# Kernel tuning notes

Hardware: AMD Instinct MI355X
Metric: run time of the kernel (lower is better)

## Reference

```python
import jax, jax.numpy as jnp
import numpy as np

P = 4            # parallel_layers
OUT_PER = 1024   # out_features // parallel_layers
IN_F = 4096
OUT_F = 4096
EPS = 1e-6


def setup_inputs() -> dict:
    key = jax.random.key(0)
    ks = jax.random.split(key, 7)
    x = jax.random.normal(ks[0], (4, 2048, IN_F), dtype=jnp.float32)
    vq_weight = jax.random.normal(ks[1], (16384, P, 32), dtype=jnp.float32)
    w_dec = jax.random.normal(ks[2], (P, 32, 256), dtype=jnp.float32) * 0.05
    b_dec = jax.random.normal(ks[3], (P, 256), dtype=jnp.float32) * 0.01
    d_mean = jax.random.normal(ks[4], (P, 1), dtype=jnp.float32) * 0.01
    d_std = jax.random.uniform(ks[5], (P, 1), dtype=jnp.float32, minval=0.01, maxval=0.05)
    bias = jax.random.normal(ks[6], (OUT_F,), dtype=jnp.float32) * 0.02
    return {"x": x, "vq_weight": vq_weight, "w_dec": w_dec, "b_dec": b_dec,
            "d_mean": d_mean, "d_std": d_std, "bias": bias}


def reference(x, vq_weight, w_dec, b_dec, d_mean, d_std, bias):
    # Decoder (fused per-parallel-layer linear): (N,P,L) x (P,L,C) -> (N,P,C)
    stacked = jnp.einsum('npl,plc->npc', vq_weight, w_dec) + b_dec[None, :, :]
    # recover_weight: permute(1,0,2) -> (P, N, C) -> flatten -> denormalize
    w_flat = jnp.transpose(stacked, (1, 0, 2)).reshape(P, -1)
    w_flat = w_flat * (d_std + EPS) + d_mean
    # reshape to (P, out_per, in_features) -> (out_features, in_features)
    w_recon = w_flat.reshape(P, OUT_PER, IN_F).reshape(OUT_F, IN_F)
    # F.linear(x, w_recon, bias)
    out = jnp.einsum('bsi,oi->bso', x, w_recon) + bias
    return out
```

## Files before the change

kernel.cpp:

```cpp
#include <hip/hip_runtime.h>
#include <stdint.h>

#define M_DIM 8192
#define IN_F  4096
#define OUT_F 4096
#define P_LAY 4


typedef __attribute__((ext_vector_type(8))) short short8;
typedef __attribute__((ext_vector_type(4))) float f32x4;

__device__ inline unsigned short f2bf(float f) {
    unsigned int u = __builtin_bit_cast(unsigned int, f);
    u += 0x7fffu + ((u >> 16) & 1u);
    return (unsigned short)(u >> 16);
}

__global__ __launch_bounds__(256)
void prep_tables(const float* __restrict__ vq, const float* __restrict__ wdec,
                 const float* __restrict__ bdec,
                 unsigned short* __restrict__ vqh,
                 unsigned short* __restrict__ wdech) {
    const int b = blockIdx.x;
    if (b < 2048) {
        const int o4  = (b * 256 + threadIdx.x) * 4;
        const int p   = o4 >> 19;
        const int t   = (o4 >> 9) & 1023;
        const int l   = (o4 >> 4) & 31;
        const int i80 = o4 & 15;
        ushort4 pk;
        pk.x = f2bf(vq[((size_t)(t * 16 + i80 + 0) * 4 + p) * 32 + l]);
        pk.y = f2bf(vq[((size_t)(t * 16 + i80 + 1) * 4 + p) * 32 + l]);
        pk.z = f2bf(vq[((size_t)(t * 16 + i80 + 2) * 4 + p) * 32 + l]);
        pk.w = f2bf(vq[((size_t)(t * 16 + i80 + 3) * 4 + p) * 32 + l]);
        *(ushort4*)(vqh + o4) = pk;
    } else {
        const int g4 = ((b - 2048) * 256 + threadIdx.x) * 4;
        const int n  = g4 >> 8;
        const int c0 = g4 & 255;
        float v[4];
        #pragma unroll
        for (int jj = 0; jj < 4; jj++) {
            if      (n < 128)  v[jj] = wdec[g4 + jj];
            else if (n < 132)  v[jj] = bdec[(n - 128) * 256 + c0 + jj];
            else if (n == 132) v[jj] = 1.0f;
            else               v[jj] = 0.0f;
        }
        ushort4 pk;
        pk.x = f2bf(v[0]); pk.y = f2bf(v[1]); pk.z = f2bf(v[2]); pk.w = f2bf(v[3]);
        *(ushort4*)(wdech + g4) = pk;
    }
}

__global__ __launch_bounds__(256)
void gen_y(const float* __restrict__ x, const unsigned short* __restrict__ wdech,
           const float* __restrict__ dmean, const float* __restrict__ dstd,
           unsigned short* __restrict__ y,
           float* __restrict__ rowterm) {
    const int tid  = threadIdx.x;
    const int lane = tid & 63;
    const int wave = tid >> 6;
    const int s = blockIdx.x * 4 + wave;

    const float* xr = x + (size_t)s * IN_F + (lane & 15) * 256 + (lane >> 4) * 8;
    short8 a[8];
    #pragma unroll
    for (int kc = 0; kc < 8; kc++) {
        float4 u = *(const float4*)(xr + kc * 32);
        float4 v = *(const float4*)(xr + kc * 32 + 4);
        short8 t;
        t[0] = (short)f2bf(u.x); t[1] = (short)f2bf(u.y);
        t[2] = (short)f2bf(u.z); t[3] = (short)f2bf(u.w);
        t[4] = (short)f2bf(v.x); t[5] = (short)f2bf(v.y);
        t[6] = (short)f2bf(v.z); t[7] = (short)f2bf(v.w);
        a[kc] = t;
    }

    const unsigned short* wrow = wdech + (lane & 15) * 256 + (lane >> 4) * 8;
    f32x4 acc[9] = {};
    #pragma unroll
    for (int kc = 0; kc < 8; kc++) {
        #pragma unroll
        for (int nt = 0; nt < 9; nt++) {
            short8 bfr = *(const short8*)(wrow + nt * 16 * 256 + kc * 32);
            acc[nt] = __builtin_amdgcn_mfma_f32_16x16x32_bf16(a[kc], bfr, acc[nt], 0, 0, 0);
        }
    }

    #pragma unroll
    for (int nt = 0; nt < 8; nt++) {
        ushort4 pk;
        pk.x = f2bf(acc[nt][0]); pk.y = f2bf(acc[nt][1]);
        pk.z = f2bf(acc[nt][2]); pk.w = f2bf(acc[nt][3]);
        const size_t off = ((size_t)((nt >> 1) * M_DIM + s) * 512)
                         + (nt & 1) * 256 + (lane & 15) * 16 + (lane >> 4) * 4;
        *(ushort4*)(y + off) = pk;
    }
    float cs = acc[8][0] + acc[8][1] + acc[8][2] + acc[8][3];
    cs += __shfl_xor(cs, 16);
    cs += __shfl_xor(cs, 32);
    const float xsum = __shfl(cs, 4);
    if (lane < 4)
        rowterm[s * 4 + lane] = (dstd[lane] + 1e-6f) * cs + dmean[lane] * xsum;
}

__device__ inline void async16(const void* g, void* l) {
    __builtin_amdgcn_global_load_lds(
        (const __attribute__((address_space(1))) void*)g,
        (__attribute__((address_space(3))) void*)l, 16, 0, 0);
}

__global__ __launch_bounds__(256, 4)
void gemm_y(const unsigned short* __restrict__ Y,
            const unsigned short* __restrict__ V,
            const float* __restrict__ rowterm,
            const float* __restrict__ dstd,
            const float* __restrict__ bias,
            float* __restrict__ C) {
    __shared__ __attribute__((aligned(16))) unsigned short sA[2 * 128 * 32];
    __shared__ __attribute__((aligned(16))) unsigned short sB[2 * 128 * 32];

    const int tid  = threadIdx.x;
    const int lane = tid & 63;
    const int wave = tid >> 6;
    const int wm = (wave >> 1) * 64;
    const int wn = (wave & 1) * 64;

    const int m0 = blockIdx.x * 128;
    const int n0 = blockIdx.y * 128;
    const int p  = n0 >> 10;
    const int t0 = n0 & 1023;

    const char* gAb = (const char*)(Y + (size_t)p * M_DIM * 512);
    const char* gBb = (const char*)(V + (size_t)p * 1024  * 512);

    f32x4 acc[4][4] = {};
    for (int k0 = 0; k0 < 512; k0 += 64) {
        __syncthreads();
        #pragma unroll
        for (int q = 0; q < 4; q++) {
            const int u      = wave * 4 + q;
            const int kc     = u >> 3;
            const int rowblk = (u & 7) * 16;
            const int row    = rowblk + (lane >> 2);
            const int cb     = (lane & 3) * 16;
            const size_t gofs = (size_t)k0 * 2 + kc * 64 + cb;
            char* ldst = (char*)sA + kc * 8192 + rowblk * 64 + lane * 16;
            async16(gAb + (size_t)(m0 + row) * 1024 + gofs, ldst);
            ldst = (char*)sB + kc * 8192 + rowblk * 64 + lane * 16;
            async16(gBb + (size_t)(t0 + row) * 1024 + gofs, ldst);
        }
        __syncthreads();

        #pragma unroll
        for (int kc = 0; kc < 2; kc++) {
            short8 bv[4];
            #pragma unroll
            for (int ni = 0; ni < 4; ni++)
                bv[ni] = *(const short8*)((const char*)sB + kc * 8192
                        + (wn + ni * 16 + (lane & 15)) * 64 + (lane >> 4) * 16);
            #pragma unroll
            for (int mi = 0; mi < 4; mi++) {
                short8 av = *(const short8*)((const char*)sA + kc * 8192
                        + (wm + mi * 16 + (lane & 15)) * 64 + (lane >> 4) * 16);
                #pragma unroll
                for (int ni = 0; ni < 4; ni++)
                    acc[mi][ni] = __builtin_amdgcn_mfma_f32_16x16x32_bf16(
                        av, bv[ni], acc[mi][ni], 0, 0, 0);
            }
        }
    }

    const int fr = lane & 15;
    const int rq = (lane >> 4) * 4;
    const float sp = dstd[p] + 1e-6f;
    #pragma unroll
    for (int mi = 0; mi < 4; mi++) {
        const int mb = m0 + wm + mi * 16 + rq;
        float rt[4];
        #pragma unroll
        for (int r = 0; r < 4; r++) rt[r] = rowterm[(mb + r) * 4 + p];
        #pragma unroll
        for (int ni = 0; ni < 4; ni++) {
            const int o = n0 + wn + ni * 16 + fr;
            const float bn = bias[o];
            float* cp = C + (size_t)mb * OUT_F + o;
            #pragma unroll
            for (int r = 0; r < 4; r++)
                cp[(size_t)r * OUT_F] = acc[mi][ni][r] * sp + rt[r] + bn;
        }
    }
}

extern "C" void kernel_launch(void* const* d_in, const int* in_sizes, int n_in,
                              void* d_out, int out_size, void* d_ws, size_t ws_size,
                              hipStream_t stream) {
    const float* x     = (const float*)d_in[0];
    const float* vq    = (const float*)d_in[1];
    const float* wdec  = (const float*)d_in[2];
    const float* bdec  = (const float*)d_in[3];
    const float* dmean = (const float*)d_in[4];
    const float* dstd  = (const float*)d_in[5];
    const float* bias  = (const float*)d_in[6];
    float* out = (float*)d_out;

    unsigned short* y     = (unsigned short*)d_ws;
    unsigned short* vqh   = y + (size_t)4 * M_DIM * 512;
    unsigned short* wdech = vqh + (size_t)4 * 1024 * 512;
    float* rowterm = (float*)(wdech + 144 * 256);

    prep_tables<<<2084, 256, 0, stream>>>(vq, wdec, bdec, vqh, wdech);
    gen_y<<<M_DIM / 4, 256, 0, stream>>>(x, wdech, dmean, dstd, y, rowterm);
    gemm_y<<<dim3(M_DIM / 128, OUT_F / 128), 256, 0, stream>>>(
        y, vqh, rowterm, dstd, bias, out);
}
```

Measured before the change: 351.0 us.

## Stage decoder weights in swizzled LDS and process four rows per wave in gen_y

gen_y now loads the first 128 rows of the bf16 decoder table into shared memory once per block with an XOR swizzle. Each wave then computes four x-rows instead of one, reusing every B fragment across four MFMA rows. This cuts repeated global loads of the weight table and makes each block do more work, so the grid shrinks to a quarter. The costs are 64KB of LDS per block and a 4x9 accumulator array that raises register pressure, which limits occupancy and latency hiding on the x loads.

```diff
diff --git a/kernel.cpp b/kernel.cpp
--- a/kernel.cpp
+++ b/kernel.cpp
@@ -52,56 +52,83 @@
     }
 }
 
-__global__ __launch_bounds__(256)
+__global__ __launch_bounds__(256, 2)
 void gen_y(const float* __restrict__ x, const unsigned short* __restrict__ wdech,
            const float* __restrict__ dmean, const float* __restrict__ dstd,
            unsigned short* __restrict__ y,
            float* __restrict__ rowterm) {
+    __shared__ __attribute__((aligned(16))) unsigned short sW[32768];
+
     const int tid  = threadIdx.x;
     const int lane = tid & 63;
     const int wave = tid >> 6;
-    const int s = blockIdx.x * 4 + wave;
-
-    const float* xr = x + (size_t)s * IN_F + (lane & 15) * 256 + (lane >> 4) * 8;
-    short8 a[8];
+    const int fr   = lane & 15;
+    const int kg   = lane >> 4;
+
     #pragma unroll
-    for (int kc = 0; kc < 8; kc++) {
-        float4 u = *(const float4*)(xr + kc * 32);
-        float4 v = *(const float4*)(xr + kc * 32 + 4);
-        short8 t;
-        t[0] = (short)f2bf(u.x); t[1] = (short)f2bf(u.y);
-        t[2] = (short)f2bf(u.z); t[3] = (short)f2bf(u.w);
-        t[4] = (short)f2bf(v.x); t[5] = (short)f2bf(v.y);
-        t[6] = (short)f2bf(v.z); t[7] = (short)f2bf(v.w);
-        a[kc] = t;
-    }
-
-    const unsigned short* wrow = wdech + (lane & 15) * 256 + (lane >> 4) * 8;
-    f32x4 acc[9] = {};
+    for (int it = 0; it < 16; ++it) {
+        const int byte = (it * 256 + tid) * 16;
+        const int n    = byte >> 9;
+        const int swz  = byte ^ ((n & 7) << 4);
+        *(int4*)((char*)sW + swz) = *(const int4*)((const char*)wdech + byte);
+    }
+    __syncthreads();
+
+    const int sb = blockIdx.x * 16 + wave * 4;
+    const float* xbase = x + (size_t)sb * IN_F + fr * 256 + kg * 8;
+    const int bswz = (fr & 7) << 4;
+
+    f32x4 acc[4][9] = {};
+    #pragma unroll 2
+    for (int kc = 0; kc < 8; ++kc) {
+        short8 a[4];
+        #pragma unroll
+        for (int mi = 0; mi < 4; ++mi) {
+            const float* xp = xbase + (size_t)mi * IN_F + kc * 32;
+            float4 u = *(const float4*)(xp);
+            float4 v = *(const float4*)(xp + 4);
+            short8 t;
+            t[0] = (short)f2bf(u.x); t[1] = (short)f2bf(u.y);
+            t[2] = (short)f2bf(u.z); t[3] = (short)f2bf(u.w);
+            t[4] = (short)f2bf(v.x); t[5] = (short)f2bf(v.y);
+            t[6] = (short)f2bf(v.z); t[7] = (short)f2bf(v.w);
+            a[mi] = t;
+        }
+        short8 b[9];
+        #pragma unroll
+        for (int nt = 0; nt < 8; ++nt) {
+            const int byte = ((nt * 16 + fr) * 512 + kc * 64 + kg * 16) ^ bswz;
+            b[nt] = *(const short8*)((const char*)sW + byte);
+        }
+        b[8] = *(const short8*)(wdech + (size_t)(128 + fr) * 256 + kc * 32 + kg * 8);
+        #pragma unroll
+        for (int mi = 0; mi < 4; ++mi) {
+            #pragma unroll
+            for (int nt = 0; nt < 9; ++nt)
+                acc[mi][nt] = __builtin_amdgcn_mfma_f32_16x16x32_bf16(
+                    a[mi], b[nt], acc[mi][nt], 0, 0, 0);
+        }
+    }
+
     #pragma unroll
-    for (int kc = 0; kc < 8; kc++) {
-        #pragma unroll
-        for (int nt = 0; nt < 9; nt++) {
-            short8 bfr = *(const short8*)(wrow + nt * 16 * 256 + kc * 32);
-            acc[nt] = __builtin_amdgcn_mfma_f32_16x16x32_bf16(a[kc], bfr, acc[nt], 0, 0, 0);
-        }
-    }
-
-    #pragma unroll
-    for (int nt = 0; nt < 8; nt++) {
-        ushort4 pk;
-        pk.x = f2bf(acc[nt][0]); pk.y = f2bf(acc[nt][1]);
-        pk.z = f2bf(acc[nt][2]); pk.w = f2bf(acc[nt][3]);
-        const size_t off = ((size_t)((nt >> 1) * M_DIM + s) * 512)
-                         + (nt & 1) * 256 + (lane & 15) * 16 + (lane >> 4) * 4;
-        *(ushort4*)(y + off) = pk;
-    }
-    float cs = acc[8][0] + acc[8][1] + acc[8][2] + acc[8][3];
-    cs += __shfl_xor(cs, 16);
-    cs += __shfl_xor(cs, 32);
-    const float xsum = __shfl(cs, 4);
-    if (lane < 4)
-        rowterm[s * 4 + lane] = (dstd[lane] + 1e-6f) * cs + dmean[lane] * xsum;
+    for (int mi = 0; mi < 4; ++mi) {
+        const int s = sb + mi;
+        #pragma unroll
+        for (int nt = 0; nt < 8; ++nt) {
+            ushort4 pk;
+            pk.x = f2bf(acc[mi][nt][0]); pk.y = f2bf(acc[mi][nt][1]);
+            pk.z = f2bf(acc[mi][nt][2]); pk.w = f2bf(acc[mi][nt][3]);
+            const size_t off = ((size_t)((nt >> 1) * M_DIM + s) * 512)
+                             + (nt & 1) * 256 + fr * 16 + kg * 4;
+            *(ushort4*)(y + off) = pk;
+        }
+        float cs = acc[mi][8][0] + acc[mi][8][1] + acc[mi][8][2] + acc[mi][8][3];
+        cs += __shfl_xor(cs, 16);
+        cs += __shfl_xor(cs, 32);
+        const float xsum = __shfl(cs, 4);
+        if (lane < 4)
+            rowterm[s * 4 + lane] = (dstd[lane] + 1e-6f) * cs + dmean[lane] * xsum;
+    }
 }
 
 __device__ inline void async16(const void* g, void* l) {
@@ -210,7 +237,7 @@
     float* rowterm = (float*)(wdech + 144 * 256);
 
     prep_tables<<<2084, 256, 0, stream>>>(vq, wdec, bdec, vqh, wdech);
-    gen_y<<<M_DIM / 4, 256, 0, stream>>>(x, wdech, dmean, dstd, y, rowterm);
+    gen_y<<<M_DIM / 16, 256, 0, stream>>>(x, wdech, dmean, dstd, y, rowterm);
     gemm_y<<<dim3(M_DIM / 128, OUT_F / 128), 256, 0, stream>>>(
         y, vqh, rowterm, dstd, bias, out);
 }
```

Result: faster. 312.7 us (-10.9%).
